# Optimization experiments

Measured on AMD Instinct MI355X. Metric: run time of the kernel, lower is better.

The kernel has to match this reference:

```python
import jax, jax.numpy as jnp
import numpy as np

D_MODEL = 1024
N_HEADS = 16
N_LAYERS = 4
N_LEVELS = 8
B, T = 2, 1024
EPS = 1e-5
ADALN_K = 0.1
ADALN_C = 2.0
FMAX = float(np.finfo(np.float32).max)


def setup_inputs() -> dict:
    key = jax.random.key(0)
    ks = jax.random.split(key, 12)
    d, L = D_MODEL, N_LAYERS
    x = jax.random.normal(ks[0], (B, T, d), dtype=jnp.float32)
    # ragged lengths -> padding mask (1 valid, 0 pad), shape (b, t, 1)
    lengths = jnp.array([T, (3 * T) // 4], dtype=jnp.int32)
    m = (jnp.arange(T)[None, :] < lengths[:, None]).astype(jnp.float32)[..., None]
    l = jax.random.randint(ks[1], (B,), 0, N_LEVELS, dtype=jnp.int32)
    s = 0.02
    Wqkv = jax.random.normal(ks[2], (L, d, 3 * d), dtype=jnp.float32) * s
    Wout = jax.random.normal(ks[3], (L, d, d), dtype=jnp.float32) * s
    bout = jnp.zeros((L, d), dtype=jnp.float32)
    adaln_attn = jax.random.normal(ks[4], (L, N_LEVELS, 2 * d), dtype=jnp.float32) * s
    adaln_ffn = jax.random.normal(ks[5], (L, N_LEVELS, 2 * d), dtype=jnp.float32) * s
    W1 = jax.random.normal(ks[6], (L, d, 4 * d), dtype=jnp.float32) * s
    b1 = jnp.zeros((L, 4 * d), dtype=jnp.float32)
    W2 = jax.random.normal(ks[7], (L, 4 * d, d), dtype=jnp.float32) * s
    b2 = jnp.zeros((L, d), dtype=jnp.float32)
    return dict(x=x, m=m, l=l, Wqkv=Wqkv, Wout=Wout, bout=bout,
                adaln_attn=adaln_attn, adaln_ffn=adaln_ffn,
                W1=W1, b1=b1, W2=W2, b2=b2)


def _adaln(x, emb, l):
    # emb: (n_levels, 2d); l: (b,)
    g = emb[l][:, None, :]                      # (b, 1, 2d)
    loggamma, beta = jnp.split(g, 2, axis=-1)
    mu = jnp.mean(x, axis=-1, keepdims=True)
    var = jnp.mean((x - mu) ** 2, axis=-1, keepdims=True)
    h = (x - mu) * jax.lax.rsqrt(var + EPS)
    h = ADALN_C * (1.0 - jax.lax.stop_gradient(ADALN_K * h)) * h
    return jnp.exp(loggamma) * h + beta


def _attention(x, m, Wqkv, Wout, bout):
    b, t, d = x.shape
    h = N_HEADS
    dh = d // h
    qkv = x @ Wqkv                               # (b, t, 3d)
    q, k, v = jnp.split(qkv, 3, axis=-1)
    q = q.reshape(b, t, h, dh)
    k = k.reshape(b, t, h, dh)
    v = v.reshape(b, t, h, dh)
    e = jnp.einsum('bihd,bjhd->bijh', q, k) * (dh ** -0.5)
    kpm = m[:, None, :, :] * m[:, :, None, :]    # (b, i, j, 1)
    causal = jnp.tril(jnp.ones((t, t), dtype=kpm.dtype))[None, :, :, None]
    kpm = kpm * causal
    e = jnp.where(kpm == 0, -FMAX, e)
    a = jax.nn.softmax(e, axis=2)                # softmax over j (dim=2), matches custom softmax
    o = jnp.einsum('bijh,bjhd->bihd', a, v).reshape(b, t, d)
    o = o @ Wout + bout
    return o * m


def reference(x, m, l, Wqkv, Wout, bout, adaln_attn, adaln_ffn, W1, b1, W2, b2):
    for i in range(N_LAYERS):
        # attention sub-block (PrenormResidual with AdaLN, requires_mask=True)
        h = _adaln(x, adaln_attn[i], l) * m
        x = (x + _attention(h, m, Wqkv[i], Wout[i], bout[i])) * m
        # FFN sub-block
        h = _adaln(x, adaln_ffn[i], l) * m
        ff = jax.nn.gelu(h @ W1[i] + b1[i], approximate=False) @ W2[i] + b2[i]
        x = (x + ff) * m
    return x
```

## Files before the change

### kernel.cpp

```cpp
#include <hip/hip_runtime.h>

#define D_MODEL 1024
#define N_HEADS 16
#define DH 64
#define N_LAYERS 4
#define N_LEVELS 8
#define BB 2
#define TT 1024
#define MM (BB*TT)
#define EPSV 1e-5f

typedef float f32x4 __attribute__((ext_vector_type(4)));
typedef short bf16x8 __attribute__((ext_vector_type(8)));

__device__ __forceinline__ float bf2f(unsigned short u) {
    union { unsigned int i; float f; } c; c.i = ((unsigned int)u) << 16; return c.f;
}
__device__ __forceinline__ unsigned short f2bf(float f) {
    union { float f; unsigned int i; } c; c.f = f;
    unsigned int x = c.i;
    return (unsigned short)((x + 0x7fffu + ((x >> 16) & 1u)) >> 16);
}
__device__ __forceinline__ float cvt_in(const void* src, long long j, int isbf) {
    return isbf ? bf2f(((const unsigned short*)src)[j]) : ((const float*)src)[j];
}

__device__ __forceinline__ void gl_lds16(const unsigned short* g, unsigned short* l) {
    __builtin_amdgcn_global_load_lds(
        (const __attribute__((address_space(1))) unsigned int*)g,
        (__attribute__((address_space(3))) unsigned int*)l,
        16, 0, 0);
}

__global__ void detect_kernel(const unsigned short* __restrict__ x, int* __restrict__ flag) {
    __shared__ int cnts[256];
    int cnt = 0;
    for (int i = threadIdx.x; i < 16384; i += 256) {
        unsigned short u = x[2 * i];
        int e = (u >> 7) & 0xFF;
        if (e >= 110 && e <= 140) cnt++;
    }
    cnts[threadIdx.x] = cnt;
    __syncthreads();
    for (int s = 128; s; s >>= 1) {
        if (threadIdx.x < s) cnts[threadIdx.x] += cnts[threadIdx.x + s];
        __syncthreads();
    }
    if (threadIdx.x == 0) flag[0] = (cnts[0] > 12000) ? 1 : 0;
}

__global__ void load_f32_kernel(const void* __restrict__ src, float* __restrict__ dst,
                                const int* __restrict__ flag, int n) {
    int i = blockIdx.x * 256 + threadIdx.x;
    if (i >= n) return;
    dst[i] = cvt_in(src, i, flag[0]);
}
__global__ void store_out_kernel(const float* __restrict__ src, void* __restrict__ dst,
                                 const int* __restrict__ flag, int n) {
    int i = blockIdx.x * 256 + threadIdx.x;
    if (i >= n) return;
    if (flag[0]) ((unsigned short*)dst)[i] = f2bf(src[i]);
    else         ((float*)dst)[i] = src[i];
}
__global__ void load_small_kernel(const void* m_in, const void* aa, const void* af_,
                                  const void* bo, const void* b1, const void* b2,
                                  float* mf, float* embA, float* embF,
                                  float* boutf, float* b1f, float* b2f,
                                  const int* __restrict__ flag) {
    int i = blockIdx.x * 256 + threadIdx.x;
    int isbf = flag[0];
    if (i < 2048)        mf[i] = cvt_in(m_in, i, isbf);
    else if (i < 67584)  embA[i - 2048] = cvt_in(aa, i - 2048, isbf);
    else if (i < 133120) embF[i - 67584] = cvt_in(af_, i - 67584, isbf);
    else if (i < 137216) boutf[i - 133120] = cvt_in(bo, i - 133120, isbf);
    else if (i < 153600) b1f[i - 137216] = cvt_in(b1, i - 137216, isbf);
    else if (i < 157696) b2f[i - 153600] = cvt_in(b2, i - 153600, isbf);
}

__global__ __launch_bounds__(256)
void transpose_layer_kernel(const void* Wqkv, const void* Wo, const void* W1, const void* W2,
                            unsigned short* wq, unsigned short* wo,
                            unsigned short* w1, unsigned short* w2,
                            const int* __restrict__ flag,
                            long long o_qkv, long long o_o, long long o_1, long long o_2) {
    __shared__ float tile[32][33];
    int bid = blockIdx.x;
    const void* src; unsigned short* dst; long long off; int N, K, nt, kt;
    if (bid < 3072)      { int t = bid;        src = Wqkv; dst = wq; off = o_qkv; N = 3072; K = 1024; nt = t % 96;  kt = t / 96; }
    else if (bid < 4096) { int t = bid - 3072; src = Wo;   dst = wo; off = o_o;   N = 1024; K = 1024; nt = t % 32;  kt = t / 32; }
    else if (bid < 8192) { int t = bid - 4096; src = W1;   dst = w1; off = o_1;   N = 4096; K = 1024; nt = t % 128; kt = t / 128; }
    else                 { int t = bid - 8192; src = W2;   dst = w2; off = o_2;   N = 1024; K = 4096; nt = t % 32;  kt = t / 32; }
    int n0 = nt * 32, k0 = kt * 32;
    int r = threadIdx.x >> 5, c = threadIdx.x & 31;
    int isbf = flag[0];
    #pragma unroll
    for (int rr = 0; rr < 4; ++rr) {
        int k = k0 + r + rr * 8;
        tile[r + rr * 8][c] = cvt_in(src, off + (long long)k * N + n0 + c, isbf);
    }
    __syncthreads();
    #pragma unroll
    for (int rr = 0; rr < 4; ++rr) {
        int n = n0 + r + rr * 8;
        dst[(size_t)n * K + k0 + c] = f2bf(tile[c][r + rr * 8]);
    }
}

__device__ __forceinline__ float blk_sum256(float v, float* red) {
    #pragma unroll
    for (int off = 32; off; off >>= 1) v += __shfl_down(v, off, 64);
    int tid = threadIdx.x;
    __syncthreads();
    if ((tid & 63) == 0) red[tid >> 6] = v;
    __syncthreads();
    return red[0] + red[1] + red[2] + red[3];
}

__global__ __launch_bounds__(256)
void adaln_kernel(const float* __restrict__ x,
                  const float* __restrict__ emb,
                  const int* __restrict__ lvl,
                  const float* __restrict__ mvec,
                  unsigned short* __restrict__ h) {
    __shared__ float red[4];
    int row = blockIdx.x;
    int b = row / TT;
    int tid = threadIdx.x;
    const float* xr = x + (size_t)row * D_MODEL;

    float s = 0.f;
    for (int j = tid; j < D_MODEL; j += 256) s += xr[j];
    float mu = blk_sum256(s, red) * (1.0f / D_MODEL);

    float vs = 0.f;
    for (int j = tid; j < D_MODEL; j += 256) { float d = xr[j] - mu; vs += d * d; }
    float var = blk_sum256(vs, red) * (1.0f / D_MODEL);
    float rstd = rsqrtf(var + EPSV);

    int lv = lvl[b];
    const float* g = emb + (size_t)lv * (2 * D_MODEL);
    float mval = mvec[row];
    unsigned short* hr = h + (size_t)row * D_MODEL;
    for (int j = tid; j < D_MODEL; j += 256) {
        float hn = (xr[j] - mu) * rstd;
        float h2 = 2.0f * (1.0f - 0.1f * hn) * hn;
        float o = __expf(g[j]) * h2 + g[D_MODEL + j];
        hr[j] = f2bf(o * mval);
    }
}

#define EPI_STORE 0
#define EPI_GELU  1
#define EPI_RESID 2
#define EPI_PART  3

template<int MI, int NI, int WR, int WC>
__global__ __launch_bounds__(512)
void gemm8_kernel(const unsigned short* __restrict__ A, int lda,
                  const unsigned short* __restrict__ BT, int ldb,
                  const float* __restrict__ bias,
                  unsigned short* __restrict__ outb,
                  const float* __restrict__ xin,
                  float* __restrict__ xout,
                  const float* __restrict__ mvec,
                  float* __restrict__ pbuf,
                  int M, int N, int K, int mode) {
    constexpr int BM = WR * MI * 16;
    constexpr int BN = WC * NI * 16;
    __shared__ __align__(16) unsigned short As[BM * 32];
    __shared__ __align__(16) unsigned short Bs[BN * 32];
    int tid = threadIdx.x;
    int wave = tid >> 6;
    int lane = tid & 63;
    int quad = lane >> 4;
    int l16  = lane & 15;
    int tileM = blockIdx.y * BM;
    int tileN = blockIdx.x * BN;
    int wm = (wave % WR) * MI * 16;
    int wn = (wave / WR) * NI * 16;

    f32x4 acc[MI][NI] = {};

    long long zoff = (long long)blockIdx.z * K;
    const unsigned short* Abase = A  + zoff + (size_t)(tileM + wave * 16 + (lane >> 2)) * lda + (lane & 3) * 8;
    const unsigned short* Bbase = BT + zoff + (size_t)(tileN + (wave % (BN / 16)) * 16 + (lane >> 2)) * ldb + (lane & 3) * 8;

    for (int k0 = 0; k0 < K; k0 += 32) {
        gl_lds16(Abase + k0, &As[wave * 512]);
        if (wave < BN / 16) gl_lds16(Bbase + k0, &Bs[wave * 512]);
        __syncthreads();

        bf16x8 af[MI], bf[NI];
        #pragma unroll
        for (int mi = 0; mi < MI; ++mi)
            af[mi] = *(const bf16x8*)(&As[(wm + mi * 16 + l16) * 32 + quad * 8]);
        #pragma unroll
        for (int ni = 0; ni < NI; ++ni)
            bf[ni] = *(const bf16x8*)(&Bs[(wn + ni * 16 + l16) * 32 + quad * 8]);
        #pragma unroll
        for (int mi = 0; mi < MI; ++mi)
            #pragma unroll
            for (int ni = 0; ni < NI; ++ni)
                acc[mi][ni] = __builtin_amdgcn_mfma_f32_16x16x32_bf16(af[mi], bf[ni], acc[mi][ni], 0, 0, 0);
        __syncthreads();
    }

    #pragma unroll
    for (int mi = 0; mi < MI; ++mi)
    #pragma unroll
    for (int ni = 0; ni < NI; ++ni) {
        #pragma unroll
        for (int r = 0; r < 4; ++r) {
            int row = tileM + wm + mi * 16 + quad * 4 + r;
            int col = tileN + wn + ni * 16 + l16;
            float v = acc[mi][ni][r];
            size_t idx = (size_t)row * N + col;
            if (mode == EPI_STORE) {
                outb[idx] = f2bf(v);
            } else if (mode == EPI_GELU) {
                v += bias[col];
                float gel = 0.5f * v * (1.0f + erff(v * 0.70710678118654752f));
                outb[idx] = f2bf(gel);
            } else if (mode == EPI_RESID) {
                v += bias[col];
                xout[idx] = (xin[idx] + v) * mvec[row];
            } else {
                pbuf[(size_t)blockIdx.z * M * N + idx] = v;
            }
        }
    }
}

__global__ void combine2_kernel(float* __restrict__ xf,
                                const float* __restrict__ pbuf,
                                const float* __restrict__ bias,
                                const float* __restrict__ mvec, int n) {
    int i = blockIdx.x * 256 + threadIdx.x;
    if (i >= n) return;
    int row = i >> 10, col = i & 1023;
    xf[i] = (xf[i] + pbuf[i] + pbuf[n + i] + bias[col]) * mvec[row];
}

#define FA_DPAD 72

__global__ __launch_bounds__(256)
void fattn_kernel(const unsigned short* __restrict__ qkv,
                  unsigned short* __restrict__ o) {
    __shared__ __align__(16) unsigned short Qs[64 * FA_DPAD];
    __shared__ __align__(16) unsigned short Ks[64 * FA_DPAD];
    __shared__ __align__(16) unsigned short Vs[64 * FA_DPAD];
    __shared__ __align__(16) unsigned short Ps[64 * FA_DPAD];

    int qt  = blockIdx.x;
    int hd  = blockIdx.y;
    int b   = blockIdx.z;
    int tid = threadIdx.x;
    int wave = tid >> 6;
    int lane = tid & 63;
    int quad = lane >> 4;
    int l16  = lane & 15;

    const unsigned short* base = qkv + (size_t)b * TT * 3072;

    {
        int r = tid >> 2, c = (tid & 3) * 16;
        const unsigned short* src = base + (size_t)(qt * 64 + r) * 3072 + hd * DH + c;
        *(uint4*)(&Qs[r * FA_DPAD + c])     = *(const uint4*)(src);
        *(uint4*)(&Qs[r * FA_DPAD + c + 8]) = *(const uint4*)(src + 8);
    }
    __syncthreads();

    bf16x8 aq[2];
    #pragma unroll
    for (int cc = 0; cc < 2; ++cc)
        aq[cc] = *(const bf16x8*)(&Qs[(wave * 16 + l16) * FA_DPAD + cc * 32 + quad * 8]);

    f32x4 Oacc[4] = {};
    float mstate[4], lstate[4];
    #pragma unroll
    for (int r = 0; r < 4; ++r) { mstate[r] = -1e30f; lstate[r] = 0.f; }

    for (int jt = 0; jt <= qt; ++jt) {
        __syncthreads();
        {
            int r = tid >> 2, c = (tid & 3) * 16;
            const unsigned short* src = base + (size_t)(jt * 64 + r) * 3072 + 1024 + hd * DH + c;
            *(uint4*)(&Ks[r * FA_DPAD + c])     = *(const uint4*)(src);
            *(uint4*)(&Ks[r * FA_DPAD + c + 8]) = *(const uint4*)(src + 8);
        }
        {
            int j = lane, c = wave * 16;
            const unsigned short* src = base + (size_t)(jt * 64 + j) * 3072 + 2048 + hd * DH + c;
            unsigned short tmp[16];
            *(uint4*)(tmp)     = *(const uint4*)(src);
            *(uint4*)(tmp + 8) = *(const uint4*)(src + 8);
            #pragma unroll
            for (int d = 0; d < 16; ++d) Vs[(c + d) * FA_DPAD + j] = tmp[d];
        }
        __syncthreads();

        f32x4 S[4] = {};
        #pragma unroll
        for (int t = 0; t < 4; ++t)
            #pragma unroll
            for (int cc = 0; cc < 2; ++cc) {
                bf16x8 bk = *(const bf16x8*)(&Ks[(t * 16 + l16) * FA_DPAD + cc * 32 + quad * 8]);
                S[t] = __builtin_amdgcn_mfma_f32_16x16x32_bf16(aq[cc], bk, S[t], 0, 0, 0);
            }

        int qrow0 = qt * 64 + wave * 16 + quad * 4;
        bool diag = (jt == qt);
        float mnew[4];
        #pragma unroll
        for (int r = 0; r < 4; ++r) {
            float v = -1e30f;
            #pragma unroll
            for (int t = 0; t < 4; ++t) {
                float s = S[t][r] * 0.125f;
                if (diag) {
                    int j = jt * 64 + t * 16 + l16;
                    if (j > qrow0 + r) s = -1e30f;
                }
                S[t][r] = s;
                v = fmaxf(v, s);
            }
            v = fmaxf(v, __shfl_xor(v, 1, 64));
            v = fmaxf(v, __shfl_xor(v, 2, 64));
            v = fmaxf(v, __shfl_xor(v, 4, 64));
            v = fmaxf(v, __shfl_xor(v, 8, 64));
            mnew[r] = fmaxf(mstate[r], v);
        }

        #pragma unroll
        for (int r = 0; r < 4; ++r) {
            float rs = 0.f;
            #pragma unroll
            for (int t = 0; t < 4; ++t) {
                float p = __expf(S[t][r] - mnew[r]);
                rs += p;
                Ps[(wave * 16 + quad * 4 + r) * FA_DPAD + t * 16 + l16] = f2bf(p);
            }
            rs += __shfl_xor(rs, 1, 64);
            rs += __shfl_xor(rs, 2, 64);
            rs += __shfl_xor(rs, 4, 64);
            rs += __shfl_xor(rs, 8, 64);
            float alpha = __expf(mstate[r] - mnew[r]);
            lstate[r] = alpha * lstate[r] + rs;
            mstate[r] = mnew[r];
            #pragma unroll
            for (int t = 0; t < 4; ++t) Oacc[t][r] *= alpha;
        }

        #pragma unroll
        for (int cc = 0; cc < 2; ++cc) {
            bf16x8 ap = *(const bf16x8*)(&Ps[(wave * 16 + l16) * FA_DPAD + cc * 32 + quad * 8]);
            #pragma unroll
            for (int t = 0; t < 4; ++t) {
                bf16x8 bv = *(const bf16x8*)(&Vs[(t * 16 + l16) * FA_DPAD + cc * 32 + quad * 8]);
                Oacc[t] = __builtin_amdgcn_mfma_f32_16x16x32_bf16(ap, bv, Oacc[t], 0, 0, 0);
            }
        }
    }

    #pragma unroll
    for (int r = 0; r < 4; ++r) {
        float inv = 1.0f / lstate[r];
        int qi = qt * 64 + wave * 16 + quad * 4 + r;
        unsigned short* orow = o + (size_t)(b * TT + qi) * D_MODEL + hd * DH;
        #pragma unroll
        for (int t = 0; t < 4; ++t)
            orow[t * 16 + l16] = f2bf(Oacc[t][r] * inv);
    }
}

#define MB (1048576u)
#define WS_FLAG   0u
#define WS_MF     4096u
#define WS_EMBA   (WS_MF + 8192u)
#define WS_EMBF   (WS_EMBA + 262144u)
#define WS_BOUT   (WS_EMBF + 262144u)
#define WS_B1     (WS_BOUT + 16384u)
#define WS_B2     (WS_B1 + 65536u)
#define WS_XF     (1u*MB)
#define WS_H      (9u*MB)
#define WS_QKV    (13u*MB)
#define WS_OB     (25u*MB)
#define WS_PART   (9u*MB)
#define WS_FF1    (29u*MB)
#define WS_WQKV   (45u*MB)
#define WS_WOUT   (51u*MB)
#define WS_W1     (53u*MB)
#define WS_W2     (61u*MB)

extern "C" void kernel_launch(void* const* d_in, const int* in_sizes, int n_in,
                              void* d_out, int out_size, void* d_ws, size_t ws_size,
                              hipStream_t stream) {
    const void* x_in  = d_in[0];
    const void* m_in  = d_in[1];
    const int*  l_in  = (const int*)d_in[2];
    const void* Wqkv  = d_in[3];
    const void* Wout  = d_in[4];
    const void* boutp = d_in[5];
    const void* ada_a = d_in[6];
    const void* ada_f = d_in[7];
    const void* W1    = d_in[8];
    const void* b1    = d_in[9];
    const void* W2    = d_in[10];
    const void* b2    = d_in[11];

    char* ws = (char*)d_ws;
    int*            flag = (int*)(ws + WS_FLAG);
    float*          mf   = (float*)(ws + WS_MF);
    float*          embA = (float*)(ws + WS_EMBA);
    float*          embF = (float*)(ws + WS_EMBF);
    float*          boutf= (float*)(ws + WS_BOUT);
    float*          b1f  = (float*)(ws + WS_B1);
    float*          b2f  = (float*)(ws + WS_B2);
    float*          xf   = (float*)(ws + WS_XF);
    unsigned short* h    = (unsigned short*)(ws + WS_H);
    unsigned short* qkv  = (unsigned short*)(ws + WS_QKV);
    unsigned short* ob   = (unsigned short*)(ws + WS_OB);
    float*          part = (float*)(ws + WS_PART);
    unsigned short* ff1  = (unsigned short*)(ws + WS_FF1);
    unsigned short* wqkvt= (unsigned short*)(ws + WS_WQKV);
    unsigned short* woutt= (unsigned short*)(ws + WS_WOUT);
    unsigned short* w1t  = (unsigned short*)(ws + WS_W1);
    unsigned short* w2t  = (unsigned short*)(ws + WS_W2);

    const int n = MM * D_MODEL;

    detect_kernel<<<1, 256, 0, stream>>>((const unsigned short*)x_in, flag);
    load_f32_kernel<<<n / 256, 256, 0, stream>>>(x_in, xf, flag, n);
    load_small_kernel<<<(157696 + 255) / 256, 256, 0, stream>>>(
        m_in, ada_a, ada_f, boutp, b1, b2, mf, embA, embF, boutf, b1f, b2f, flag);

    const long long nqkv = (long long)D_MODEL * 3 * D_MODEL;
    const long long nsq  = (long long)D_MODEL * D_MODEL;
    const long long nw1  = (long long)D_MODEL * 4 * D_MODEL;

    for (int i = 0; i < N_LAYERS; ++i) {
        transpose_layer_kernel<<<12288, 256, 0, stream>>>(
            Wqkv, Wout, W1, W2, wqkvt, woutt, w1t, w2t, flag,
            i * nqkv, i * nsq, i * nw1, i * nw1);

        adaln_kernel<<<MM, 256, 0, stream>>>(xf, embA + (size_t)i * N_LEVELS * 2 * D_MODEL, l_in, mf, h);
        gemm8_kernel<4,2,2,4><<<dim3(3072 / 128, MM / 128), 512, 0, stream>>>(
            h, 1024, wqkvt, 1024, nullptr, qkv, nullptr, nullptr, nullptr, nullptr,
            MM, 3072, 1024, EPI_STORE);
        fattn_kernel<<<dim3(TT / 64, N_HEADS, BB), 256, 0, stream>>>(qkv, ob);
        gemm8_kernel<2,2,4,2><<<dim3(1024 / 64, MM / 128), 512, 0, stream>>>(
            ob, 1024, woutt, 1024, boutf + (size_t)i * D_MODEL, nullptr, xf, xf, mf, nullptr,
            MM, 1024, 1024, EPI_RESID);
        adaln_kernel<<<MM, 256, 0, stream>>>(xf, embF + (size_t)i * N_LEVELS * 2 * D_MODEL, l_in, mf, h);
        gemm8_kernel<4,2,2,4><<<dim3(4096 / 128, MM / 128), 512, 0, stream>>>(
            h, 1024, w1t, 1024, b1f + (size_t)i * 4 * D_MODEL, ff1, nullptr, nullptr, nullptr, nullptr,
            MM, 4096, 1024, EPI_GELU);
        gemm8_kernel<2,2,4,2><<<dim3(1024 / 64, MM / 128, 2), 512, 0, stream>>>(
            ff1, 4096, w2t, 4096, nullptr, nullptr, nullptr, nullptr, nullptr, part,
            MM, 1024, 2048, EPI_PART);
        combine2_kernel<<<n / 256, 256, 0, stream>>>(
            xf, part, b2f + (size_t)i * D_MODEL, mf, n);
    }

    store_out_kernel<<<n / 256, 256, 0, stream>>>(xf, d_out, flag, n);
}
```

Baseline: 1.057 ms.

## Split attention KV loop across two blocks, fuse output store and single-pass AdaLN stats

Causal flash attention now has two blocks per query tile, each taking alternating key tiles. Each block writes fp32 partial outputs plus its running max and sum, and a new merge kernel combines the two and writes bf16. This gives more blocks and shortens the longest per-block loop on the causal workload, at the cost of extra fp32 traffic and one more launch. The final store kernel is folded into the last combine2 launch. AdaLN mean and variance are now computed in a single pass using E[x^2]-mu^2, which can lose precision.

Measured after the change: 1.021 ms. 3.4% less time.

```diff
diff --git a/kernel.cpp b/kernel.cpp
--- a/kernel.cpp
+++ b/kernel.cpp
@@ -54,13 +54,6 @@
     int i = blockIdx.x * 256 + threadIdx.x;
     if (i >= n) return;
     dst[i] = cvt_in(src, i, flag[0]);
-}
-__global__ void store_out_kernel(const float* __restrict__ src, void* __restrict__ dst,
-                                 const int* __restrict__ flag, int n) {
-    int i = blockIdx.x * 256 + threadIdx.x;
-    if (i >= n) return;
-    if (flag[0]) ((unsigned short*)dst)[i] = f2bf(src[i]);
-    else         ((float*)dst)[i] = src[i];
 }
 __global__ void load_small_kernel(const void* m_in, const void* aa, const void* af_,
                                   const void* bo, const void* b1, const void* b2,
@@ -106,14 +99,18 @@
     }
 }
 
-__device__ __forceinline__ float blk_sum256(float v, float* red) {
-    #pragma unroll
-    for (int off = 32; off; off >>= 1) v += __shfl_down(v, off, 64);
+__device__ __forceinline__ void blk_sum2_256(float& a, float& b, float* red) {
+    #pragma unroll
+    for (int off = 32; off; off >>= 1) {
+        a += __shfl_down(a, off, 64);
+        b += __shfl_down(b, off, 64);
+    }
     int tid = threadIdx.x;
     __syncthreads();
-    if ((tid & 63) == 0) red[tid >> 6] = v;
+    if ((tid & 63) == 0) { red[tid >> 6] = a; red[4 + (tid >> 6)] = b; }
     __syncthreads();
-    return red[0] + red[1] + red[2] + red[3];
+    a = red[0] + red[1] + red[2] + red[3];
+    b = red[4] + red[5] + red[6] + red[7];
 }
 
 __global__ __launch_bounds__(256)
@@ -122,19 +119,17 @@
                   const int* __restrict__ lvl,
                   const float* __restrict__ mvec,
                   unsigned short* __restrict__ h) {
-    __shared__ float red[4];
+    __shared__ float red[8];
     int row = blockIdx.x;
     int b = row / TT;
     int tid = threadIdx.x;
     const float* xr = x + (size_t)row * D_MODEL;
 
-    float s = 0.f;
-    for (int j = tid; j < D_MODEL; j += 256) s += xr[j];
-    float mu = blk_sum256(s, red) * (1.0f / D_MODEL);
-
-    float vs = 0.f;
-    for (int j = tid; j < D_MODEL; j += 256) { float d = xr[j] - mu; vs += d * d; }
-    float var = blk_sum256(vs, red) * (1.0f / D_MODEL);
+    float s = 0.f, ss = 0.f;
+    for (int j = tid; j < D_MODEL; j += 256) { float v = xr[j]; s += v; ss += v * v; }
+    blk_sum2_256(s, ss, red);
+    float mu = s * (1.0f / D_MODEL);
+    float var = ss * (1.0f / D_MODEL) - mu * mu;
     float rstd = rsqrtf(var + EPSV);
 
     int lv = lvl[b];
@@ -234,18 +229,26 @@
 __global__ void combine2_kernel(float* __restrict__ xf,
                                 const float* __restrict__ pbuf,
                                 const float* __restrict__ bias,
-                                const float* __restrict__ mvec, int n) {
+                                const float* __restrict__ mvec,
+                                void* __restrict__ outp,
+                                const int* __restrict__ flag, int n) {
     int i = blockIdx.x * 256 + threadIdx.x;
     if (i >= n) return;
     int row = i >> 10, col = i & 1023;
-    xf[i] = (xf[i] + pbuf[i] + pbuf[n + i] + bias[col]) * mvec[row];
+    float v = (xf[i] + pbuf[i] + pbuf[n + i] + bias[col]) * mvec[row];
+    xf[i] = v;
+    if (outp) {
+        if (flag[0]) ((unsigned short*)outp)[i] = f2bf(v);
+        else         ((float*)outp)[i] = v;
+    }
 }
 
 #define FA_DPAD 72
 
 __global__ __launch_bounds__(256)
-void fattn_kernel(const unsigned short* __restrict__ qkv,
-                  unsigned short* __restrict__ o) {
+void fattn_split_kernel(const unsigned short* __restrict__ qkv,
+                        float* __restrict__ Opart,
+                        float* __restrict__ ml) {
     __shared__ __align__(16) unsigned short Qs[64 * FA_DPAD];
     __shared__ __align__(16) unsigned short Ks[64 * FA_DPAD];
     __shared__ __align__(16) unsigned short Vs[64 * FA_DPAD];
@@ -253,7 +256,8 @@
 
     int qt  = blockIdx.x;
     int hd  = blockIdx.y;
-    int b   = blockIdx.z;
+    int b   = blockIdx.z >> 1;
+    int s   = blockIdx.z & 1;
     int tid = threadIdx.x;
     int wave = tid >> 6;
     int lane = tid & 63;
@@ -280,7 +284,7 @@
     #pragma unroll
     for (int r = 0; r < 4; ++r) { mstate[r] = -1e30f; lstate[r] = 0.f; }
 
-    for (int jt = 0; jt <= qt; ++jt) {
+    for (int jt = s; jt <= qt; jt += 2) {
         __syncthreads();
         {
             int r = tid >> 2, c = (tid & 3) * 16;
@@ -316,13 +320,13 @@
             float v = -1e30f;
             #pragma unroll
             for (int t = 0; t < 4; ++t) {
-                float s = S[t][r] * 0.125f;
+                float sv = S[t][r] * 0.125f;
                 if (diag) {
                     int j = jt * 64 + t * 16 + l16;
-                    if (j > qrow0 + r) s = -1e30f;
+                    if (j > qrow0 + r) sv = -1e30f;
                 }
-                S[t][r] = s;
-                v = fmaxf(v, s);
+                S[t][r] = sv;
+                v = fmaxf(v, sv);
             }
             v = fmaxf(v, __shfl_xor(v, 1, 64));
             v = fmaxf(v, __shfl_xor(v, 2, 64));
@@ -364,13 +368,35 @@
 
     #pragma unroll
     for (int r = 0; r < 4; ++r) {
-        float inv = 1.0f / lstate[r];
         int qi = qt * 64 + wave * 16 + quad * 4 + r;
-        unsigned short* orow = o + (size_t)(b * TT + qi) * D_MODEL + hd * DH;
+        size_t row = (size_t)b * TT + qi;
+        float* orow = Opart + (size_t)s * MM * D_MODEL + row * D_MODEL + hd * DH;
         #pragma unroll
         for (int t = 0; t < 4; ++t)
-            orow[t * 16 + l16] = f2bf(Oacc[t][r] * inv);
-    }
+            orow[t * 16 + l16] = Oacc[t][r];
+        if (l16 == 0) {
+            float* mlp = ml + (((size_t)s * MM + row) * N_HEADS + hd) * 2;
+            mlp[0] = mstate[r];
+            mlp[1] = lstate[r];
+        }
+    }
+}
+
+__global__ void attn_merge_kernel(const float* __restrict__ Opart,
+                                  const float* __restrict__ ml,
+                                  unsigned short* __restrict__ ob) {
+    int i = blockIdx.x * 256 + threadIdx.x;
+    int row = i >> 10;
+    int hd  = (i >> 6) & 15;
+    const float* ml0 = ml + (((size_t)row) * N_HEADS + hd) * 2;
+    const float* ml1 = ml + (((size_t)MM + row) * N_HEADS + hd) * 2;
+    float m0 = ml0[0], l0 = ml0[1];
+    float m1 = ml1[0], l1 = ml1[1];
+    float M = fmaxf(m0, m1);
+    float w0 = __expf(m0 - M), w1 = __expf(m1 - M);
+    float den = w0 * l0 + w1 * l1;
+    float num = w0 * Opart[i] + w1 * Opart[(size_t)MM * D_MODEL + i];
+    ob[i] = f2bf(num / den);
 }
 
 #define MB (1048576u)
@@ -386,7 +412,9 @@
 #define WS_QKV    (13u*MB)
 #define WS_OB     (25u*MB)
 #define WS_PART   (9u*MB)
+#define WS_ML     (9u*MB)
 #define WS_FF1    (29u*MB)
+#define WS_OPART  (29u*MB)
 #define WS_WQKV   (45u*MB)
 #define WS_WOUT   (51u*MB)
 #define WS_W1     (53u*MB)
@@ -421,6 +449,8 @@
     unsigned short* qkv  = (unsigned short*)(ws + WS_QKV);
     unsigned short* ob   = (unsigned short*)(ws + WS_OB);
     float*          part = (float*)(ws + WS_PART);
+    float*          mlb  = (float*)(ws + WS_ML);
+    float*          opart= (float*)(ws + WS_OPART);
     unsigned short* ff1  = (unsigned short*)(ws + WS_FF1);
     unsigned short* wqkvt= (unsigned short*)(ws + WS_WQKV);
     unsigned short* woutt= (unsigned short*)(ws + WS_WOUT);
@@ -447,7 +477,8 @@
         gemm8_kernel<4,2,2,4><<<dim3(3072 / 128, MM / 128), 512, 0, stream>>>(
             h, 1024, wqkvt, 1024, nullptr, qkv, nullptr, nullptr, nullptr, nullptr,
             MM, 3072, 1024, EPI_STORE);
-        fattn_kernel<<<dim3(TT / 64, N_HEADS, BB), 256, 0, stream>>>(qkv, ob);
+        fattn_split_kernel<<<dim3(TT / 64, N_HEADS, BB * 2), 256, 0, stream>>>(qkv, opart, mlb);
+        attn_merge_kernel<<<n / 256, 256, 0, stream>>>(opart, mlb, ob);
         gemm8_kernel<2,2,4,2><<<dim3(1024 / 64, MM / 128), 512, 0, stream>>>(
             ob, 1024, woutt, 1024, boutf + (size_t)i * D_MODEL, nullptr, xf, xf, mf, nullptr,
             MM, 1024, 1024, EPI_RESID);
@@ -459,8 +490,7 @@
             ff1, 4096, w2t, 4096, nullptr, nullptr, nullptr, nullptr, nullptr, part,
             MM, 1024, 2048, EPI_PART);
         combine2_kernel<<<n / 256, 256, 0, stream>>>(
-            xf, part, b2f + (size_t)i * D_MODEL, mf, n);
-    }
-
-    store_out_kernel<<<n / 256, 256, 0, stream>>>(xf, d_out, flag, n);
-}
+            xf, part, b2f + (size_t)i * D_MODEL, mf,
+            (i == N_LAYERS - 1) ? d_out : nullptr, flag, n);
+    }
+}
```
